# Performance work log

Measured on AMD Instinct MI355X. Metric: run time of the kernel, lower is better.

## Reference

```python
import jax, jax.numpy as jnp
import numpy as np

# Config constants (mirror EnergyConfig)
MIN_CARD = 26.0
CARD_PEN = 25.0
PLANE_W = 1.0
FACET_W = 8.0
RANK_EPS = 1e-6
BOUND_W = 4.0
SUP_W = 1.0
ACT_W = 1.0
INACT_W = 0.35
MARGIN = 0.05
PROB_POW = 1.0
PLANE_TOPK = 128
ACTIVE_TOPK = 64

N_POINTS, DIM, BATCH = 65536, 8, 256


def _topk_filter(w, k):
    # Keep only the top-k entries per row, zero elsewhere (scatter of gathered values).
    if k <= 0 or k >= w.shape[-1]:
        return w
    vals, idx = jax.lax.top_k(w, k)
    rows = jnp.arange(w.shape[0])[:, None]
    return jnp.zeros_like(w).at[rows, idx].set(vals)


def setup_inputs() -> dict:
    key = jax.random.key(0)
    k1, k2 = jax.random.split(key)
    probabilities = jax.random.uniform(k1, (BATCH, N_POINTS), dtype=jnp.float32)
    points = jax.random.normal(k2, (N_POINTS, DIM), dtype=jnp.float32)
    return {"probabilities": probabilities, "points": points}


def reference(probabilities, points):
    prob = jnp.clip(probabilities, 1e-5, 1.0 - 1e-5)  # (B,N)

    # ---- weighted plane statistics (weighted PCA) ----
    pw = _topk_filter(prob, PLANE_TOPK)                       # (B,N)
    wsum = jnp.clip(pw.sum(-1), 1e-6)                          # (B,)
    mean = (pw @ points) / wsum[:, None]                       # (B,D)
    pp = points[:, :, None] * points[:, None, :]               # (N,D,D), small since D=8
    second_moment = jnp.einsum('bn,nij->bij', pw, pp) / wsum[:, None, None]
    cov = second_moment - mean[:, :, None] * mean[:, None, :]  # (B,D,D)
    cov = 0.5 * (cov + cov.swapaxes(1, 2))
    eigvals, eigvecs = jnp.linalg.eigh(cov)                    # ascending
    plane_term = eigvals[:, 0]
    second_eig = eigvals[:, 1]
    facet_term = plane_term / (second_eig + RANK_EPS)
    normal = eigvecs[:, :, 0]                                  # (B,D) smallest-eig direction

    # ---- dual-orientation boundary terms ----
    proj = points @ normal.T                                   # (N,B)
    active_w = _topk_filter(prob ** PROB_POW, ACTIVE_TOPK)     # (B,N)
    active_norm = jnp.clip(active_w.sum(-1), 1e-6)
    inactive_w = 1.0 - prob
    inactive_norm = jnp.clip(inactive_w.sum(-1), 1e-6)

    def orientation_boundary(p):
        # p: (N,B) oriented projections
        offset = -p.max(axis=0)                                # (B,)
        signed = p + offset[None, :]                           # (N,B), max is 0
        sb = signed.T                                          # (B,N)
        active_res = sb * sb                                   # quadratic active loss
        active = (active_w * active_res).sum(-1) / active_norm
        slack = jax.nn.relu(MARGIN + sb)
        inactive = (inactive_w * slack * slack).sum(-1) / inactive_norm
        support = jax.nn.relu(signed.max(axis=0)) ** 2
        return SUP_W * support + ACT_W * active + INACT_W * inactive

    b_pos = orientation_boundary(proj)
    b_neg = orientation_boundary(-proj)
    boundary = jnp.where(b_pos <= b_neg, b_pos, b_neg)

    # ---- cardinality penalty ----
    cardinality = prob.sum(-1)
    deficit = jax.nn.relu(MIN_CARD - cardinality)
    card_term = CARD_PEN * deficit * deficit

    total = PLANE_W * plane_term + FACET_W * facet_term + BOUND_W * boundary + card_term
    return total
```

## Files before the change

### kernel.cpp

```cpp
#include <hip/hip_runtime.h>
#include <cstdint>
#include <cstddef>

constexpr int NPTS   = 65536;
constexpr int B      = 256;
constexpr int CHUNKS = 8;
constexpr int CHUNK  = NPTS / CHUNKS;
constexpr int CCAP   = 256;
constexpr int NBLK   = B * CHUNKS;
constexpr int NEARCAP = 128;

constexpr size_t WSO_CBUF    = 0;
constexpr size_t WSO_NEAR    = WSO_CBUF + (size_t)NBLK * CCAP * 2;
constexpr size_t WSO_NEARCNT = WSO_NEAR + (size_t)2 * B * NEARCAP * 2;
constexpr size_t WSO_PSUM    = WSO_NEARCNT + 2 * B;
constexpr size_t WSO_CCNT    = WSO_PSUM + NBLK;
constexpr size_t WSO_PLANE   = WSO_CCNT + NBLK;
constexpr size_t WSO_FACET   = WSO_PLANE + B;
constexpr size_t WSO_NRM     = WSO_FACET + B;
constexpr size_t WSO_SUMP    = WSO_NRM + (size_t)B * 8;
constexpr size_t WSO_ANORM   = WSO_SUMP + B;
constexpr size_t WSO_T64V    = WSO_ANORM + B;
constexpr size_t WSO_T64I    = WSO_T64V + (size_t)B * 64;
constexpr size_t WSO_PMAXP   = WSO_T64I + (size_t)B * 64;
constexpr size_t WSO_PMAXN   = WSO_PMAXP + B;

__device__ __forceinline__ float clipp(float x) {
    return fminf(fmaxf(x, 1e-5f), 0.99999f);
}
__device__ __forceinline__ unsigned f2mono(float f) {
    unsigned u = __float_as_uint(f);
    return (u & 0x80000000u) ? ~u : (u | 0x80000000u);
}
__device__ __forceinline__ float mono2f(unsigned e) {
    return __uint_as_float((e & 0x80000000u) ? (e ^ 0x80000000u) : ~e);
}
__device__ __forceinline__ int cand_bin(float v) {
    int b = (int)((v - 0.99f) * 102400.0f);
    return min(max(b, 0), 1023);
}
__device__ __forceinline__ float dot8(float4 a, float4 b, const float* n) {
    float d = a.x * n[0];
    d = fmaf(a.y, n[1], d); d = fmaf(a.z, n[2], d); d = fmaf(a.w, n[3], d);
    d = fmaf(b.x, n[4], d); d = fmaf(b.y, n[5], d); d = fmaf(b.z, n[6], d);
    d = fmaf(b.w, n[7], d);
    return d;
}

__global__ __launch_bounds__(256) void kA_stream(
    const float* __restrict__ prob, float* __restrict__ ws)
{
    __shared__ float wred[4];
    __shared__ int lcnt;
    const int tid   = threadIdx.x;
    const int row   = blockIdx.x >> 3;
    const int chunk = blockIdx.x & 7;
    if (tid == 0) lcnt = 0;
    __syncthreads();

    unsigned long long* cb = (unsigned long long*)ws + (size_t)blockIdx.x * CCAP;
    const float4* p4 = (const float4*)(prob + (size_t)row * NPTS + (size_t)chunk * CHUNK);
    float lsum = 0.f;
    #pragma unroll
    for (int i = 0; i < CHUNK / 4 / 256; i++) {
        float4 v = p4[i * 256 + tid];
        float c0 = clipp(v.x), c1 = clipp(v.y), c2 = clipp(v.z), c3 = clipp(v.w);
        lsum += (c0 + c1) + (c2 + c3);
        float mx = fmaxf(fmaxf(c0, c1), fmaxf(c2, c3));
        if (mx >= 0.99f) {
            int bi = chunk * CHUNK + (i * 256 + tid) * 4;
            float c4[4] = {c0, c1, c2, c3};
            #pragma unroll
            for (int j = 0; j < 4; j++) {
                if (c4[j] >= 0.99f) {
                    int p_ = atomicAdd(&lcnt, 1);
                    if (p_ < CCAP)
                        cb[p_] = (((unsigned long long)__float_as_uint(c4[j])) << 32)
                               | (unsigned)~(bi + j);
                }
            }
        }
    }
    #pragma unroll
    for (int off = 32; off; off >>= 1) lsum += __shfl_down(lsum, off);
    if ((tid & 63) == 0) wred[tid >> 6] = lsum;
    __syncthreads();
    if (tid == 0) {
        ws[WSO_PSUM + blockIdx.x] = (wred[0] + wred[1]) + (wred[2] + wred[3]);
        ((int*)ws)[WSO_CCNT + blockIdx.x] = min(lcnt, CCAP);
    }
}

__global__ __launch_bounds__(256) void kB_select(
    const float* __restrict__ points, float* __restrict__ ws)
{
    __shared__ unsigned long long cand[CHUNKS * CCAP];
    __shared__ unsigned long long comp[256];
    __shared__ int   hist[1024];
    __shared__ int   counts_s[CHUNKS];
    __shared__ int   ccnt_s, bt_s;
    __shared__ float sw[128];
    __shared__ float pc[128][9];
    __shared__ float sred[44][4];
    __shared__ float slotm[44];
    __shared__ float wpart[2];
    __shared__ float covm[64];

    const int row = blockIdx.x;
    const int tid = threadIdx.x;

    if (tid < CHUNKS) counts_s[tid] = ((const int*)ws)[WSO_CCNT + row * CHUNKS + tid];
    if (tid == 0) { ccnt_s = 0; bt_s = 0; }
    #pragma unroll
    for (int k = 0; k < 4; k++) hist[tid * 4 + k] = 0;
    __syncthreads();

    const unsigned long long* cb = (const unsigned long long*)ws;
    #pragma unroll
    for (int r = 0; r < CHUNKS; r++) {
        int s = r * 256 + tid;
        int c = s >> 8, t = s & 255;
        unsigned long long k = 0ull;
        if (t < counts_s[c]) {
            k = cb[((size_t)(row * CHUNKS + c) << 8) + t];
            atomicAdd(&hist[cand_bin(__uint_as_float((unsigned)(k >> 32)))], 1);
        }
        cand[s] = k;
    }
    __syncthreads();

    if (tid < 64) {
        int h[16]; int g = 0;
        #pragma unroll
        for (int k = 0; k < 16; k++) { h[k] = hist[tid * 16 + k]; g += h[k]; }
        int s = g;
        #pragma unroll
        for (int off = 1; off < 64; off <<= 1) {
            int o = __shfl_down(s, off);
            if (tid + off < 64) s += o;
        }
        int Snext = __shfl_down(s, 1);
        if (tid == 63) Snext = 0;
        if (s >= 128 && Snext < 128) {
            int acc = Snext, bt = tid * 16;
            #pragma unroll
            for (int k = 15; k >= 0; k--) {
                acc += h[k];
                if (acc >= 128) { bt = tid * 16 + k; break; }
            }
            bt_s = bt;
        }
    }
    __syncthreads();

    const int bt = bt_s;
    #pragma unroll
    for (int r = 0; r < CHUNKS; r++) {
        unsigned long long k = cand[r * 256 + tid];
        if (k && cand_bin(__uint_as_float((unsigned)(k >> 32))) >= bt) {
            int p_ = atomicAdd(&ccnt_s, 1);
            if (p_ < 256) comp[p_] = k;
        }
    }
    __syncthreads();
    const int m = min(ccnt_s, 256);

    if (tid < 128) {
        sw[tid] = 0.f;
        #pragma unroll
        for (int j = 0; j < 9; j++) pc[tid][j] = (j == 8) ? 1.f : 0.f;
    }
    if (tid < 64) {
        ws[WSO_T64V + (size_t)row * 64 + tid] = 0.f;
        ((int*)ws)[WSO_T64I + (size_t)row * 64 + tid] = 0;
    }
    unsigned long long ki = (tid < m) ? comp[tid] : 0ull;
    int rank = 0;
    for (int j = 0; j < m; j++) rank += (comp[j] > ki) ? 1 : 0;
    __syncthreads();

    if (tid < m && rank < 128) {
        float v = __uint_as_float((unsigned)(ki >> 32));
        unsigned idx = ~(unsigned)(ki & 0xFFFFFFFFu);
        sw[rank] = v;
        const float4* pt = (const float4*)(points + (size_t)idx * 8);
        float4 q0 = pt[0], q1 = pt[1];
        pc[rank][0] = q0.x; pc[rank][1] = q0.y; pc[rank][2] = q0.z; pc[rank][3] = q0.w;
        pc[rank][4] = q1.x; pc[rank][5] = q1.y; pc[rank][6] = q1.z; pc[rank][7] = q1.w;
        if (rank < 64) {
            ws[WSO_T64V + (size_t)row * 64 + rank] = v;
            ((int*)ws)[WSO_T64I + (size_t)row * 64 + rank] = (int)idx;
        }
    }
    __syncthreads();

    if (tid < 128) {
        float ww = sw[tid];
        #pragma unroll
        for (int off = 32; off; off >>= 1) ww += __shfl_down(ww, off);
        if ((tid & 63) == 0) wpart[tid >> 6] = ww;
    }
    if (tid < 176) {
        int s = tid >> 2, part = tid & 3;
        int i_, j_;
        if (s < 36) {
            int rem = s; i_ = 0;
            while (rem >= 8 - i_) { rem -= 8 - i_; i_++; }
            j_ = i_ + rem;
        } else { i_ = s - 36; j_ = 8; }
        float acc = 0.f;
        for (int k = part * 32; k < part * 32 + 32; k++)
            acc += sw[k] * pc[k][i_] * pc[k][j_];
        sred[s][part] = acc;
    }
    __syncthreads();
    if (tid < 44) slotm[tid] = (sred[tid][0] + sred[tid][1]) + (sred[tid][2] + sred[tid][3]);
    __syncthreads();

    if (tid < 64) {
        float w128 = fmaxf(wpart[0] + wpart[1], 1e-6f);
        int i_ = tid >> 3, j_ = tid & 7;
        int a_ = min(i_, j_), b_ = max(i_, j_);
        int s3 = 8 * a_ - (a_ * (a_ - 1)) / 2 + (b_ - a_);
        covm[tid] = slotm[s3] / w128 - (slotm[36 + i_] / w128) * (slotm[36 + j_] / w128);
    }
    __syncthreads();

    if (tid == 64) {
        ws[WSO_ANORM + row] = fmaxf(wpart[0], 1e-6f);
        float s = 0.f;
        for (int c = 0; c < CHUNKS; c++) s += ws[WSO_PSUM + row * CHUNKS + c];
        ws[WSO_SUMP + row] = s;
        ((unsigned*)ws)[WSO_PMAXP + row] = 0u;
        ((unsigned*)ws)[WSO_PMAXN + row] = 0u;
        ((int*)ws)[WSO_NEARCNT + row * 2 + 0] = 0;
        ((int*)ws)[WSO_NEARCNT + row * 2 + 1] = 0;
    }

    if (tid < 64) {
        const int i = tid >> 3, j = tid & 7;
        float a = covm[tid];
        float v = (i == j) ? 1.f : 0.f;
        const unsigned PR[7] = {023456701u, 001234567u, 050712346u, 034067125u,
                                012305674u, 067120453u, 045671032u};
        #pragma unroll 1
        for (int sweep = 0; sweep < 6; sweep++) {
            #pragma unroll
            for (int r = 0; r < 7; r++) {
                const unsigned pk = PR[r];
                const int rp = (pk >> (3 * i)) & 7;
                const int cp = (pk >> (3 * j)) & 7;
                const int pr = min(i, rp), qr = max(i, rp);
                float app = __shfl(a, pr * 9);
                float aqq = __shfl(a, qr * 9);
                float apq = __shfl(a, pr * 8 + qr);
                float tau = 0.5f * (aqq - app);
                float den = fabsf(tau) + sqrtf(fmaf(tau, tau, apq * apq));
                float t = __fdividef(apq, den + 1e-38f);
                t = (tau < 0.f) ? -t : t;
                float cr = rsqrtf(fmaf(t, t, 1.f));
                float sr = t * cr;
                float cc = __shfl(cr, j * 9);
                float sc = __shfl(sr, j * 9);
                float oth = __shfl(a, rp * 8 + j);
                a = fmaf((i < rp) ? -sr : sr, oth, cr * a);
                float oth2 = __shfl(a, i * 8 + cp);
                a = fmaf((j < cp) ? -sc : sc, oth2, cc * a);
                float ov = __shfl(v, i * 8 + cp);
                v = fmaf((j < cp) ? -sc : sc, ov, cc * v);
            }
        }
        float d[8];
        #pragma unroll
        for (int k = 0; k < 8; k++) d[k] = __shfl(a, k * 9);
        float e0 = d[0]; int i0 = 0;
        #pragma unroll
        for (int k = 1; k < 8; k++) if (d[k] < e0) { e0 = d[k]; i0 = k; }
        float e1 = 3.4e38f;
        #pragma unroll
        for (int k = 0; k < 8; k++) if (k != i0 && d[k] < e1) e1 = d[k];
        if (tid == 0) {
            ws[WSO_PLANE + row] = e0;
            ws[WSO_FACET + row] = e0 / (e1 + 1e-6f);
        }
        if (j == i0) ws[WSO_NRM + (size_t)row * 8 + i] = v;
    }
}

constexpr int R3 = 4;
constexpr int P3 = 2048;
__global__ __launch_bounds__(256) void k3a_max(
    const float* __restrict__ points, float* __restrict__ ws)
{
    __shared__ float redp[4][R3], redn[4][R3];
    __shared__ float bmax[2 * R3];
    const int tid = threadIdx.x;
    const int r0  = blockIdx.y * R3;
    const int n0  = blockIdx.x * P3;
    float nr[R3][8];
    #pragma unroll
    for (int r = 0; r < R3; r++)
        #pragma unroll
        for (int j = 0; j < 8; j++)
            nr[r][j] = ws[WSO_NRM + (size_t)(r0 + r) * 8 + j];
    float dsv[P3 / 256][R3];
    float mp[R3], mn[R3];
    #pragma unroll
    for (int r = 0; r < R3; r++) { mp[r] = -3.4e38f; mn[r] = -3.4e38f; }
    const float4* pb = (const float4*)points + (size_t)n0 * 2;
    #pragma unroll
    for (int it = 0; it < P3 / 256; it++) {
        int t2 = (it * 256 + tid) * 2;
        float4 q0 = pb[t2], q1 = pb[t2 + 1];
        #pragma unroll
        for (int r = 0; r < R3; r++) {
            float d = dot8(q0, q1, nr[r]);
            dsv[it][r] = d;
            mp[r] = fmaxf(mp[r], d);
            mn[r] = fmaxf(mn[r], -d);
        }
    }
    #pragma unroll
    for (int r = 0; r < R3; r++) {
        #pragma unroll
        for (int off = 32; off; off >>= 1) {
            mp[r] = fmaxf(mp[r], __shfl_xor(mp[r], off));
            mn[r] = fmaxf(mn[r], __shfl_xor(mn[r], off));
        }
    }
    if ((tid & 63) == 0) {
        int wv = tid >> 6;
        #pragma unroll
        for (int r = 0; r < R3; r++) { redp[wv][r] = mp[r]; redn[wv][r] = mn[r]; }
    }
    __syncthreads();
    if (tid < 2 * R3) {
        int r = tid & (R3 - 1);
        bool neg = tid >= R3;
        float m = neg
            ? fmaxf(fmaxf(redn[0][r], redn[1][r]), fmaxf(redn[2][r], redn[3][r]))
            : fmaxf(fmaxf(redp[0][r], redp[1][r]), fmaxf(redp[2][r], redp[3][r]));
        bmax[tid] = m;
        unsigned* wsu = (unsigned*)ws;
        atomicMax(&wsu[(neg ? WSO_PMAXN : WSO_PMAXP) + r0 + r], f2mono(m));
    }
    __syncthreads();
    float bmx[R3], bmn[R3];
    #pragma unroll
    for (int r = 0; r < R3; r++) { bmx[r] = bmax[r]; bmn[r] = bmax[R3 + r]; }

    int* ncnt = (int*)ws + WSO_NEARCNT;
    unsigned long long* nbuf = (unsigned long long*)ws + WSO_NEAR / 2;
    #pragma unroll
    for (int it = 0; it < P3 / 256; it++) {
        int nn = n0 + it * 256 + tid;
        #pragma unroll
        for (int r = 0; r < R3; r++) {
            float d = dsv[it][r];
            if (d >= bmx[r] - 0.05f) {
                int p_ = atomicAdd(&ncnt[(r0 + r) * 2 + 0], 1);
                if (p_ < NEARCAP)
                    nbuf[(size_t)((r0 + r) * 2 + 0) * NEARCAP + p_] =
                        (((unsigned long long)__float_as_uint(d)) << 32) | (unsigned)nn;
            }
            if (-d >= bmn[r] - 0.05f) {
                int p_ = atomicAdd(&ncnt[(r0 + r) * 2 + 1], 1);
                if (p_ < NEARCAP)
                    nbuf[(size_t)((r0 + r) * 2 + 1) * NEARCAP + p_] =
                        (((unsigned long long)__float_as_uint(-d)) << 32) | (unsigned)nn;
            }
        }
    }
}

__global__ __launch_bounds__(64) void k3cd_final(
    const float* __restrict__ points, const float* __restrict__ prob,
    const float* __restrict__ ws, float* __restrict__ out)
{
    const int row = blockIdx.x;
    const int t   = threadIdx.x;
    const unsigned* wsu = (const unsigned*)ws;
    __shared__ float nl[8];
    if (t < 8) nl[t] = ws[WSO_NRM + (size_t)row * 8 + t];
    __syncthreads();

    const float pmaxp = mono2f(wsu[WSO_PMAXP + row]);
    const float pmaxn = mono2f(wsu[WSO_PMAXN + row]);

    float w   = ws[WSO_T64V + (size_t)row * 64 + t];
    int   idx = ((const int*)ws)[WSO_T64I + (size_t)row * 64 + t];
    const float4* pt = (const float4*)(points + (size_t)idx * 8);
    float4 q0 = pt[0], q1 = pt[1];
    float d = dot8(q0, q1, nl);
    float sp = d - pmaxp, sn = -d - pmaxn;
    float ap = w * sp * sp;
    float an = w * sn * sn;

    const int* ncnt = (const int*)ws + WSO_NEARCNT;
    const unsigned long long* nbuf = (const unsigned long long*)ws + WSO_NEAR / 2;
    float ip = 0.f, in_ = 0.f;
    int cp = min(ncnt[row * 2 + 0], NEARCAP);
    int cn = min(ncnt[row * 2 + 1], NEARCAP);
    for (int i = t; i < cp; i += 64) {
        unsigned long long e = nbuf[(size_t)(row * 2 + 0) * NEARCAP + i];
        float dv = __uint_as_float((unsigned)(e >> 32));
        float tp = 0.05f + (dv - pmaxp);
        if (tp > 0.f) {
            float w2 = 1.0f - clipp(prob[(size_t)row * NPTS + (unsigned)(e & 0xFFFFFFFFu)]);
            ip = fmaf(w2 * tp, tp, ip);
        }
    }
    for (int i = t; i < cn; i += 64) {
        unsigned long long e = nbuf[(size_t)(row * 2 + 1) * NEARCAP + i];
        float dv = __uint_as_float((unsigned)(e >> 32));
        float tn = 0.05f + (dv - pmaxn);
        if (tn > 0.f) {
            float w2 = 1.0f - clipp(prob[(size_t)row * NPTS + (unsigned)(e & 0xFFFFFFFFu)]);
            in_ = fmaf(w2 * tn, tn, in_);
        }
    }
    #pragma unroll
    for (int off = 32; off; off >>= 1) {
        ap  += __shfl_down(ap, off);
        an  += __shfl_down(an, off);
        ip  += __shfl_down(ip, off);
        in_ += __shfl_down(in_, off);
    }
    if (t == 0) {
        float anorm = ws[WSO_ANORM + row];
        float sump  = ws[WSO_SUMP + row];
        float inorm = fmaxf((float)NPTS - sump, 1e-6f);
        float bp = (ap / anorm) + 0.35f * (ip / inorm);
        float bn = (an / anorm) + 0.35f * (in_ / inorm);
        float bd = (bp <= bn) ? bp : bn;
        float def = fmaxf(26.0f - sump, 0.f);
        out[row] = ws[WSO_PLANE + row] + 8.0f * ws[WSO_FACET + row]
                 + 4.0f * bd + 25.0f * def * def;
    }
}

extern "C" void kernel_launch(void* const* d_in, const int* in_sizes, int n_in,
                              void* d_out, int out_size, void* d_ws, size_t ws_size,
                              hipStream_t stream) {
    const float* prob   = (const float*)d_in[0];
    const float* points = (const float*)d_in[1];
    float* out = (float*)d_out;
    float* ws  = (float*)d_ws;

    kA_stream<<<NBLK, 256, 0, stream>>>(prob, ws);
    kB_select<<<B, 256, 0, stream>>>(points, ws);
    dim3 g3(NPTS / P3, B / R3);
    k3a_max<<<g3, 256, 0, stream>>>(points, ws);
    k3cd_final<<<B, 64, 0, stream>>>(points, prob, ws, out);
}
```

Measured before the change: 148.3 us.

## Fuse four kernels into two using last-block-done atomic counters

```diff
diff --git a/kernel.cpp b/kernel.cpp
--- a/kernel.cpp
+++ b/kernel.cpp
@@ -2,28 +2,31 @@
 #include <cstdint>
 #include <cstddef>
 
-constexpr int NPTS   = 65536;
-constexpr int B      = 256;
-constexpr int CHUNKS = 8;
-constexpr int CHUNK  = NPTS / CHUNKS;
-constexpr int CCAP   = 256;
-constexpr int NBLK   = B * CHUNKS;
+constexpr int NPTS    = 65536;
+constexpr int B       = 256;
+constexpr int CHUNKS  = 8;
+constexpr int CHUNK   = NPTS / CHUNKS;
+constexpr int CCAP    = 256;
+constexpr int NBLK    = B * CHUNKS;
 constexpr int NEARCAP = 128;
 
 constexpr size_t WSO_CBUF    = 0;
 constexpr size_t WSO_NEAR    = WSO_CBUF + (size_t)NBLK * CCAP * 2;
-constexpr size_t WSO_NEARCNT = WSO_NEAR + (size_t)2 * B * NEARCAP * 2;
-constexpr size_t WSO_PSUM    = WSO_NEARCNT + 2 * B;
-constexpr size_t WSO_CCNT    = WSO_PSUM + NBLK;
+constexpr size_t WSO_ZERO    = WSO_NEAR + (size_t)2 * B * NEARCAP * 2;
+constexpr size_t WSO_NEARCNT = WSO_ZERO;
+constexpr size_t WSO_ROWDONE = WSO_NEARCNT + 2 * B;
+constexpr size_t WSO_R3DONE  = WSO_ROWDONE + B;
+constexpr size_t WSO_SUMP    = WSO_R3DONE + B;
+constexpr size_t WSO_PMAXP   = WSO_SUMP + B;
+constexpr size_t WSO_PMAXN   = WSO_PMAXP + B;
+constexpr size_t WSO_ZEROEND = WSO_PMAXN + B;
+constexpr size_t WSO_CCNT    = WSO_ZEROEND;
 constexpr size_t WSO_PLANE   = WSO_CCNT + NBLK;
 constexpr size_t WSO_FACET   = WSO_PLANE + B;
 constexpr size_t WSO_NRM     = WSO_FACET + B;
-constexpr size_t WSO_SUMP    = WSO_NRM + (size_t)B * 8;
-constexpr size_t WSO_ANORM   = WSO_SUMP + B;
+constexpr size_t WSO_ANORM   = WSO_NRM + (size_t)B * 8;
 constexpr size_t WSO_T64V    = WSO_ANORM + B;
 constexpr size_t WSO_T64I    = WSO_T64V + (size_t)B * 64;
-constexpr size_t WSO_PMAXP   = WSO_T64I + (size_t)B * 64;
-constexpr size_t WSO_PMAXN   = WSO_PMAXP + B;
 
 __device__ __forceinline__ float clipp(float x) {
     return fminf(fmaxf(x, 1e-5f), 0.99999f);
@@ -46,19 +49,46 @@
     d = fmaf(b.w, n[7], d);
     return d;
 }
-
-__global__ __launch_bounds__(256) void kA_stream(
-    const float* __restrict__ prob, float* __restrict__ ws)
+__device__ __forceinline__ void ast_u64(unsigned long long* p, unsigned long long v) {
+    __hip_atomic_store(p, v, __ATOMIC_RELAXED, __HIP_MEMORY_SCOPE_AGENT);
+}
+__device__ __forceinline__ unsigned long long ald_u64(const unsigned long long* p) {
+    return __hip_atomic_load(p, __ATOMIC_RELAXED, __HIP_MEMORY_SCOPE_AGENT);
+}
+__device__ __forceinline__ void ast_i32(int* p, int v) {
+    __hip_atomic_store(p, v, __ATOMIC_RELAXED, __HIP_MEMORY_SCOPE_AGENT);
+}
+__device__ __forceinline__ int ald_i32(const int* p) {
+    return __hip_atomic_load(p, __ATOMIC_RELAXED, __HIP_MEMORY_SCOPE_AGENT);
+}
+__device__ __forceinline__ unsigned ald_u32(const unsigned* p) {
+    return __hip_atomic_load(p, __ATOMIC_RELAXED, __HIP_MEMORY_SCOPE_AGENT);
+}
+
+__global__ __launch_bounds__(256) void k1_stream_select(
+    const float* __restrict__ prob, const float* __restrict__ points,
+    float* __restrict__ ws)
 {
+    __shared__ unsigned long long cand[CHUNKS * CCAP];
+    __shared__ unsigned long long comp[256];
+    __shared__ int   hist[1024];
+    __shared__ int   counts_s[CHUNKS];
+    __shared__ int   ccnt_s, bt_s, last_s, lcnt;
+    __shared__ float sw[128];
+    __shared__ float pc[128][9];
+    __shared__ float sred[44][4];
+    __shared__ float slotm[44];
+    __shared__ float wpart[2];
+    __shared__ float covm[64];
     __shared__ float wred[4];
-    __shared__ int lcnt;
+
     const int tid   = threadIdx.x;
     const int row   = blockIdx.x >> 3;
     const int chunk = blockIdx.x & 7;
     if (tid == 0) lcnt = 0;
     __syncthreads();
 
-    unsigned long long* cb = (unsigned long long*)ws + (size_t)blockIdx.x * CCAP;
+    unsigned long long* cb0 = (unsigned long long*)ws + (size_t)blockIdx.x * CCAP;
     const float4* p4 = (const float4*)(prob + (size_t)row * NPTS + (size_t)chunk * CHUNK);
     float lsum = 0.f;
     #pragma unroll
@@ -75,8 +105,9 @@
                 if (c4[j] >= 0.99f) {
                     int p_ = atomicAdd(&lcnt, 1);
                     if (p_ < CCAP)
-                        cb[p_] = (((unsigned long long)__float_as_uint(c4[j])) << 32)
-                               | (unsigned)~(bi + j);
+                        ast_u64(&cb0[p_],
+                            (((unsigned long long)__float_as_uint(c4[j])) << 32)
+                            | (unsigned)~(bi + j));
                 }
             }
         }
@@ -86,30 +117,16 @@
     if ((tid & 63) == 0) wred[tid >> 6] = lsum;
     __syncthreads();
     if (tid == 0) {
-        ws[WSO_PSUM + blockIdx.x] = (wred[0] + wred[1]) + (wred[2] + wred[3]);
-        ((int*)ws)[WSO_CCNT + blockIdx.x] = min(lcnt, CCAP);
-    }
-}
-
-__global__ __launch_bounds__(256) void kB_select(
-    const float* __restrict__ points, float* __restrict__ ws)
-{
-    __shared__ unsigned long long cand[CHUNKS * CCAP];
-    __shared__ unsigned long long comp[256];
-    __shared__ int   hist[1024];
-    __shared__ int   counts_s[CHUNKS];
-    __shared__ int   ccnt_s, bt_s;
-    __shared__ float sw[128];
-    __shared__ float pc[128][9];
-    __shared__ float sred[44][4];
-    __shared__ float slotm[44];
-    __shared__ float wpart[2];
-    __shared__ float covm[64];
-
-    const int row = blockIdx.x;
-    const int tid = threadIdx.x;
-
-    if (tid < CHUNKS) counts_s[tid] = ((const int*)ws)[WSO_CCNT + row * CHUNKS + tid];
+        atomicAdd(&ws[WSO_SUMP + row], (wred[0] + wred[1]) + (wred[2] + wred[3]));
+        ast_i32((int*)ws + WSO_CCNT + blockIdx.x, min(lcnt, CCAP));
+        int old = __hip_atomic_fetch_add((int*)ws + WSO_ROWDONE + row, 1,
+                                         __ATOMIC_ACQ_REL, __HIP_MEMORY_SCOPE_AGENT);
+        last_s = (old == CHUNKS - 1);
+    }
+    __syncthreads();
+    if (!last_s) return;
+
+    if (tid < CHUNKS) counts_s[tid] = ald_i32((int*)ws + WSO_CCNT + row * CHUNKS + tid);
     if (tid == 0) { ccnt_s = 0; bt_s = 0; }
     #pragma unroll
     for (int k = 0; k < 4; k++) hist[tid * 4 + k] = 0;
@@ -122,7 +139,7 @@
         int c = s >> 8, t = s & 255;
         unsigned long long k = 0ull;
         if (t < counts_s[c]) {
-            k = cb[((size_t)(row * CHUNKS + c) << 8) + t];
+            k = ald_u64(&cb[((size_t)(row * CHUNKS + c) << 8) + t]);
             atomicAdd(&hist[cand_bin(__uint_as_float((unsigned)(k >> 32)))], 1);
         }
         cand[s] = k;
@@ -224,18 +241,8 @@
         int s3 = 8 * a_ - (a_ * (a_ - 1)) / 2 + (b_ - a_);
         covm[tid] = slotm[s3] / w128 - (slotm[36 + i_] / w128) * (slotm[36 + j_] / w128);
     }
-    __syncthreads();
-
-    if (tid == 64) {
-        ws[WSO_ANORM + row] = fmaxf(wpart[0], 1e-6f);
-        float s = 0.f;
-        for (int c = 0; c < CHUNKS; c++) s += ws[WSO_PSUM + row * CHUNKS + c];
-        ws[WSO_SUMP + row] = s;
-        ((unsigned*)ws)[WSO_PMAXP + row] = 0u;
-        ((unsigned*)ws)[WSO_PMAXN + row] = 0u;
-        ((int*)ws)[WSO_NEARCNT + row * 2 + 0] = 0;
-        ((int*)ws)[WSO_NEARCNT + row * 2 + 1] = 0;
-    }
+    if (tid == 64) ws[WSO_ANORM + row] = fmaxf(wpart[0], 1e-6f);
+    __syncthreads();
 
     if (tid < 64) {
         const int i = tid >> 3, j = tid & 7;
@@ -289,11 +296,13 @@
 
 constexpr int R3 = 4;
 constexpr int P3 = 2048;
-__global__ __launch_bounds__(256) void k3a_max(
-    const float* __restrict__ points, float* __restrict__ ws)
+__global__ __launch_bounds__(256) void k2_max_final(
+    const float* __restrict__ points, const float* __restrict__ prob,
+    float* __restrict__ ws, float* __restrict__ out)
 {
     __shared__ float redp[4][R3], redn[4][R3];
     __shared__ float bmax[2 * R3];
+    __shared__ int   flag[R3];
     const int tid = threadIdx.x;
     const int r0  = blockIdx.y * R3;
     const int n0  = blockIdx.x * P3;
@@ -360,82 +369,79 @@
             if (d >= bmx[r] - 0.05f) {
                 int p_ = atomicAdd(&ncnt[(r0 + r) * 2 + 0], 1);
                 if (p_ < NEARCAP)
-                    nbuf[(size_t)((r0 + r) * 2 + 0) * NEARCAP + p_] =
-                        (((unsigned long long)__float_as_uint(d)) << 32) | (unsigned)nn;
+                    ast_u64(&nbuf[(size_t)((r0 + r) * 2 + 0) * NEARCAP + p_],
+                        (((unsigned long long)__float_as_uint(d)) << 32) | (unsigned)nn);
             }
             if (-d >= bmn[r] - 0.05f) {
                 int p_ = atomicAdd(&ncnt[(r0 + r) * 2 + 1], 1);
                 if (p_ < NEARCAP)
-                    nbuf[(size_t)((r0 + r) * 2 + 1) * NEARCAP + p_] =
-                        (((unsigned long long)__float_as_uint(-d)) << 32) | (unsigned)nn;
-            }
-        }
-    }
-}
-
-__global__ __launch_bounds__(64) void k3cd_final(
-    const float* __restrict__ points, const float* __restrict__ prob,
-    const float* __restrict__ ws, float* __restrict__ out)
-{
-    const int row = blockIdx.x;
-    const int t   = threadIdx.x;
+                    ast_u64(&nbuf[(size_t)((r0 + r) * 2 + 1) * NEARCAP + p_],
+                        (((unsigned long long)__float_as_uint(-d)) << 32) | (unsigned)nn);
+            }
+        }
+    }
+    __syncthreads();
+    if (tid < R3) {
+        int old = __hip_atomic_fetch_add((int*)ws + WSO_R3DONE + r0 + tid, 1,
+                                         __ATOMIC_ACQ_REL, __HIP_MEMORY_SCOPE_AGENT);
+        flag[tid] = (old == (NPTS / P3) - 1) ? 1 : 0;
+    }
+    __syncthreads();
+    if (tid >= 64) return;
+    const int t = tid;
     const unsigned* wsu = (const unsigned*)ws;
-    __shared__ float nl[8];
-    if (t < 8) nl[t] = ws[WSO_NRM + (size_t)row * 8 + t];
-    __syncthreads();
-
-    const float pmaxp = mono2f(wsu[WSO_PMAXP + row]);
-    const float pmaxn = mono2f(wsu[WSO_PMAXN + row]);
-
-    float w   = ws[WSO_T64V + (size_t)row * 64 + t];
-    int   idx = ((const int*)ws)[WSO_T64I + (size_t)row * 64 + t];
-    const float4* pt = (const float4*)(points + (size_t)idx * 8);
-    float4 q0 = pt[0], q1 = pt[1];
-    float d = dot8(q0, q1, nl);
-    float sp = d - pmaxp, sn = -d - pmaxn;
-    float ap = w * sp * sp;
-    float an = w * sn * sn;
-
-    const int* ncnt = (const int*)ws + WSO_NEARCNT;
-    const unsigned long long* nbuf = (const unsigned long long*)ws + WSO_NEAR / 2;
-    float ip = 0.f, in_ = 0.f;
-    int cp = min(ncnt[row * 2 + 0], NEARCAP);
-    int cn = min(ncnt[row * 2 + 1], NEARCAP);
-    for (int i = t; i < cp; i += 64) {
-        unsigned long long e = nbuf[(size_t)(row * 2 + 0) * NEARCAP + i];
-        float dv = __uint_as_float((unsigned)(e >> 32));
-        float tp = 0.05f + (dv - pmaxp);
-        if (tp > 0.f) {
-            float w2 = 1.0f - clipp(prob[(size_t)row * NPTS + (unsigned)(e & 0xFFFFFFFFu)]);
-            ip = fmaf(w2 * tp, tp, ip);
-        }
-    }
-    for (int i = t; i < cn; i += 64) {
-        unsigned long long e = nbuf[(size_t)(row * 2 + 1) * NEARCAP + i];
-        float dv = __uint_as_float((unsigned)(e >> 32));
-        float tn = 0.05f + (dv - pmaxn);
-        if (tn > 0.f) {
-            float w2 = 1.0f - clipp(prob[(size_t)row * NPTS + (unsigned)(e & 0xFFFFFFFFu)]);
-            in_ = fmaf(w2 * tn, tn, in_);
-        }
-    }
-    #pragma unroll
-    for (int off = 32; off; off >>= 1) {
-        ap  += __shfl_down(ap, off);
-        an  += __shfl_down(an, off);
-        ip  += __shfl_down(ip, off);
-        in_ += __shfl_down(in_, off);
-    }
-    if (t == 0) {
-        float anorm = ws[WSO_ANORM + row];
-        float sump  = ws[WSO_SUMP + row];
-        float inorm = fmaxf((float)NPTS - sump, 1e-6f);
-        float bp = (ap / anorm) + 0.35f * (ip / inorm);
-        float bn = (an / anorm) + 0.35f * (in_ / inorm);
-        float bd = (bp <= bn) ? bp : bn;
-        float def = fmaxf(26.0f - sump, 0.f);
-        out[row] = ws[WSO_PLANE + row] + 8.0f * ws[WSO_FACET + row]
-                 + 4.0f * bd + 25.0f * def * def;
+    for (int r = 0; r < R3; r++) {
+        if (!flag[r]) continue;
+        const int row = r0 + r;
+        const float pmaxp = mono2f(ald_u32(&wsu[WSO_PMAXP + row]));
+        const float pmaxn = mono2f(ald_u32(&wsu[WSO_PMAXN + row]));
+        float w   = ws[WSO_T64V + (size_t)row * 64 + t];
+        int   idx = ((const int*)ws)[WSO_T64I + (size_t)row * 64 + t];
+        const float4* pt = (const float4*)(points + (size_t)idx * 8);
+        float4 q0 = pt[0], q1 = pt[1];
+        float d = dot8(q0, q1, nr[r]);
+        float sp = d - pmaxp, sn = -d - pmaxn;
+        float ap = w * sp * sp;
+        float an = w * sn * sn;
+        float ip = 0.f, in_ = 0.f;
+        int cp = min(ald_i32(&ncnt[row * 2 + 0]), NEARCAP);
+        int cn = min(ald_i32(&ncnt[row * 2 + 1]), NEARCAP);
+        for (int i = t; i < cp; i += 64) {
+            unsigned long long e = ald_u64(&nbuf[(size_t)(row * 2 + 0) * NEARCAP + i]);
+            float dv = __uint_as_float((unsigned)(e >> 32));
+            float tp = 0.05f + (dv - pmaxp);
+            if (tp > 0.f) {
+                float w2 = 1.0f - clipp(prob[(size_t)row * NPTS + (unsigned)(e & 0xFFFFFFFFu)]);
+                ip = fmaf(w2 * tp, tp, ip);
+            }
+        }
+        for (int i = t; i < cn; i += 64) {
+            unsigned long long e = ald_u64(&nbuf[(size_t)(row * 2 + 1) * NEARCAP + i]);
+            float dv = __uint_as_float((unsigned)(e >> 32));
+            float tn = 0.05f + (dv - pmaxn);
+            if (tn > 0.f) {
+                float w2 = 1.0f - clipp(prob[(size_t)row * NPTS + (unsigned)(e & 0xFFFFFFFFu)]);
+                in_ = fmaf(w2 * tn, tn, in_);
+            }
+        }
+        #pragma unroll
+        for (int off = 32; off; off >>= 1) {
+            ap  += __shfl_down(ap, off);
+            an  += __shfl_down(an, off);
+            ip  += __shfl_down(ip, off);
+            in_ += __shfl_down(in_, off);
+        }
+        if (t == 0) {
+            float anorm = ws[WSO_ANORM + row];
+            float sump  = ws[WSO_SUMP + row];
+            float inorm = fmaxf((float)NPTS - sump, 1e-6f);
+            float bp = (ap / anorm) + 0.35f * (ip / inorm);
+            float bn = (an / anorm) + 0.35f * (in_ / inorm);
+            float bd = (bp <= bn) ? bp : bn;
+            float def = fmaxf(26.0f - sump, 0.f);
+            out[row] = ws[WSO_PLANE + row] + 8.0f * ws[WSO_FACET + row]
+                     + 4.0f * bd + 25.0f * def * def;
+        }
     }
 }
 
@@ -447,9 +453,9 @@
     float* out = (float*)d_out;
     float* ws  = (float*)d_ws;
 
-    kA_stream<<<NBLK, 256, 0, stream>>>(prob, ws);
-    kB_select<<<B, 256, 0, stream>>>(points, ws);
-    dim3 g3(NPTS / P3, B / R3);
-    k3a_max<<<g3, 256, 0, stream>>>(points, ws);
-    k3cd_final<<<B, 64, 0, stream>>>(points, prob, ws, out);
-}
+    hipMemsetAsync((char*)d_ws + WSO_ZERO * 4, 0,
+                   (WSO_ZEROEND - WSO_ZERO) * 4, stream);
+    k1_stream_select<<<NBLK, 256, 0, stream>>>(prob, points, ws);
+    dim3 g2(NPTS / P3, B / R3);
+    k2_max_final<<<g2, 256, 0, stream>>>(points, prob, ws, out);
+}
```

After: 254.5 us. 71.6% more time.
